# Optimization experiments

Measured on AMD Instinct MI355X. Metric: run time of the kernel, lower is better.

## Reference

```python
import jax, jax.numpy as jnp
import numpy as np

NUM_UNITS = 256
DIM_HIDDEN = 1024
NUM_GROUPS = 8
BATCH = 768
MASK_P = 0.2


def setup_inputs() -> dict:
    key = jax.random.key(0)
    k_x, k_m, k_w1, k_w2 = jax.random.split(key, 4)
    x = jax.random.normal(k_x, (BATCH, NUM_UNITS), dtype=jnp.float32)
    mask = jax.random.bernoulli(k_m, MASK_P, (BATCH, NUM_UNITS))  # True = drop unit
    # Xavier-normal initialized linear layers (zeros bias), as in _weights_init.
    s1 = float(np.sqrt(2.0 / (NUM_UNITS + DIM_HIDDEN)))
    s2 = float(np.sqrt(2.0 / (DIM_HIDDEN + NUM_UNITS)))
    W1 = jax.random.normal(k_w1, (NUM_UNITS, DIM_HIDDEN), dtype=jnp.float32) * s1
    b1 = jnp.zeros((DIM_HIDDEN,), dtype=jnp.float32)
    W2 = jax.random.normal(k_w2, (DIM_HIDDEN, NUM_UNITS), dtype=jnp.float32) * s2
    b2 = jnp.zeros((NUM_UNITS,), dtype=jnp.float32)
    temperature = jnp.ones((NUM_UNITS,), dtype=jnp.float32)
    return {"x": x, "mask": mask, "W1": W1, "b1": b1, "W2": W2, "b2": b2,
            "temperature": temperature}


def _mlp(v, W1, b1, W2, b2):
    h = jax.nn.leaky_relu(v @ W1 + b1, negative_slope=0.01)
    return h @ W2 + b2


def reference(x, mask, W1, b1, W2, b2, temperature):
    B = x.shape[0]
    key_ = _mlp(x, W1, b1, W2, b2)                      # [B, U]
    x_masked = jnp.where(mask, 0.0, x)                  # UnitMask: drop units
    query = _mlp(x_masked, W1, b1, W2, b2)              # [B, U]
    # w[i, j, u] = -|key[j,u] - query[i,u]| * temperature[u]
    w = -jnp.abs(key_[None, :, :] - query[:, None, :]) * temperature
    eye = jnp.eye(B, dtype=bool)[:, :, None]
    w = jnp.where(eye, -jnp.inf, w)
    w = w.reshape(B, B // NUM_GROUPS, NUM_GROUPS, NUM_UNITS)
    w = jax.nn.softmax(w, axis=1)
    w = w.reshape(B, B, NUM_UNITS) / 8
    return (w, mask)
```

## Files before the change

kernel.cpp:

```cpp
#include <hip/hip_runtime.h>
#include <math.h>

#define NU   256
#define DH   1024
#define NG   8
#define BB   768
#define NU4  64
#define JCH  96

typedef float nfloat4 __attribute__((ext_vector_type(4)));

__global__ __launch_bounds__(256) void build_x2(const float* __restrict__ x,
                                                const int* __restrict__ mask,
                                                float* __restrict__ X2) {
    int idx = blockIdx.x * 256 + threadIdx.x;
    int r = idx >> 8;
    int c = idx & 255;
    if (r < BB) {
        X2[idx] = x[idx];
    } else {
        int src = (r - BB) * NU + c;
        X2[idx] = mask[src] ? 0.0f : x[src];
    }
}

__global__ __launch_bounds__(256) void gemm_bias(const float* __restrict__ A,
                                                 const float* __restrict__ B,
                                                 const float* __restrict__ bias,
                                                 float* __restrict__ C,
                                                 int M, int N, int K, int leaky) {
    const int BK = 16;
    __shared__ float As[BK][64 + 1];
    __shared__ float Bs[BK][64];
    int t  = threadIdx.x;
    int tx = t & 15;
    int ty = t >> 4;
    int m0 = blockIdx.y * 64;
    int n0 = blockIdx.x * 64;

    float acc[4][4] = {};

    for (int k0 = 0; k0 < K; k0 += BK) {
        {
            int r = t >> 2;
            int c = (t & 3) * 4;
            const float4 a = *(const float4*)&A[(size_t)(m0 + r) * K + k0 + c];
            As[c + 0][r] = a.x;
            As[c + 1][r] = a.y;
            As[c + 2][r] = a.z;
            As[c + 3][r] = a.w;
        }
        {
            int r = t >> 4;
            int c = (t & 15) * 4;
            *(float4*)&Bs[r][c] = *(const float4*)&B[(size_t)(k0 + r) * N + n0 + c];
        }
        __syncthreads();
        #pragma unroll
        for (int k = 0; k < BK; ++k) {
            float a[4], b[4];
            #pragma unroll
            for (int q = 0; q < 4; ++q) a[q] = As[k][ty * 4 + q];
            #pragma unroll
            for (int q = 0; q < 4; ++q) b[q] = Bs[k][tx * 4 + q];
            #pragma unroll
            for (int im = 0; im < 4; ++im)
                #pragma unroll
                for (int in = 0; in < 4; ++in)
                    acc[im][in] = fmaf(a[im], b[in], acc[im][in]);
        }
        __syncthreads();
    }

    #pragma unroll
    for (int im = 0; im < 4; ++im) {
        int m = m0 + ty * 4 + im;
        #pragma unroll
        for (int in = 0; in < 4; ++in) {
            int n = n0 + tx * 4 + in;
            float v = acc[im][in] + bias[n];
            if (leaky) v = v > 0.0f ? v : 0.01f * v;
            C[(size_t)m * N + n] = v;
        }
    }
}

__global__ __launch_bounds__(256) void stats_kernel(const float* __restrict__ KQ,
                                                    const float* __restrict__ temp,
                                                    float* __restrict__ scale) {
    const int i  = blockIdx.x;
    const int t  = threadIdx.x;
    const int u4 = t & 63;
    const int r  = t >> 6;

    const float4* key4 = (const float4*)KQ;
    const float4* qry4 = (const float4*)(KQ + (size_t)BB * NU);
    const float4 q  = qry4[(size_t)i * NU4 + u4];
    const float4 tp = ((const float4*)temp)[u4];

    float4 sa = make_float4(0.f, 0.f, 0.f, 0.f);
    float4 sb = make_float4(0.f, 0.f, 0.f, 0.f);

    #pragma unroll 4
    for (int k = 0; k < 192; k += 2) {
        const int jA = r + 4 * k;
        const int jB = jA + 4;
        const float4 ka = key4[(size_t)jA * NU4 + u4];
        const float4 kb = key4[(size_t)jB * NU4 + u4];
        if (jA != i) {
            sa.x += __expf(-fabsf(ka.x - q.x) * tp.x);
            sa.y += __expf(-fabsf(ka.y - q.y) * tp.y);
            sa.z += __expf(-fabsf(ka.z - q.z) * tp.z);
            sa.w += __expf(-fabsf(ka.w - q.w) * tp.w);
        }
        if (jB != i) {
            sb.x += __expf(-fabsf(kb.x - q.x) * tp.x);
            sb.y += __expf(-fabsf(kb.y - q.y) * tp.y);
            sb.z += __expf(-fabsf(kb.z - q.z) * tp.z);
            sb.w += __expf(-fabsf(kb.w - q.w) * tp.w);
        }
    }

    float4 ia = make_float4(0.125f / sa.x, 0.125f / sa.y, 0.125f / sa.z, 0.125f / sa.w);
    float4 ib = make_float4(0.125f / sb.x, 0.125f / sb.y, 0.125f / sb.z, 0.125f / sb.w);
    ((float4*)scale)[((size_t)i * NG + r) * NU4 + u4]     = ia;
    ((float4*)scale)[((size_t)i * NG + r + 4) * NU4 + u4] = ib;
}

__global__ __launch_bounds__(256) void attn_write(const float* __restrict__ KQ,
                                                  const float* __restrict__ temp,
                                                  const float* __restrict__ scale,
                                                  float* __restrict__ out) {
    const int jc = blockIdx.x;
    const int i  = blockIdx.y;
    const int t  = threadIdx.x;
    const int u4 = t & 63;
    const int r  = t >> 6;
    const int j0 = jc * JCH;

    const float4* key4 = (const float4*)KQ;
    const float4* qry4 = (const float4*)(KQ + (size_t)BB * NU);
    const float4 q  = qry4[(size_t)i * NU4 + u4];
    const float4 tp = ((const float4*)temp)[u4];
    const float4 va = ((const float4*)scale)[((size_t)i * NG + r) * NU4 + u4];
    const float4 vb = ((const float4*)scale)[((size_t)i * NG + r + 4) * NU4 + u4];

    nfloat4* o4 = (nfloat4*)out + (size_t)i * BB * NU4;

    #pragma unroll 4
    for (int k = 0; k < 24; k += 2) {
        const int jA = j0 + r + 4 * k;
        const int jB = jA + 4;
        const float4 ka = key4[(size_t)jA * NU4 + u4];
        const float4 kb = key4[(size_t)jB * NU4 + u4];
        nfloat4 ea, eb;
        ea.x = __expf(-fabsf(ka.x - q.x) * tp.x) * va.x;
        ea.y = __expf(-fabsf(ka.y - q.y) * tp.y) * va.y;
        ea.z = __expf(-fabsf(ka.z - q.z) * tp.z) * va.z;
        ea.w = __expf(-fabsf(ka.w - q.w) * tp.w) * va.w;
        eb.x = __expf(-fabsf(kb.x - q.x) * tp.x) * vb.x;
        eb.y = __expf(-fabsf(kb.y - q.y) * tp.y) * vb.y;
        eb.z = __expf(-fabsf(kb.z - q.z) * tp.z) * vb.z;
        eb.w = __expf(-fabsf(kb.w - q.w) * tp.w) * vb.w;
        if (jA == i) ea = (nfloat4)0.0f;
        if (jB == i) eb = (nfloat4)0.0f;
        __builtin_nontemporal_store(ea, &o4[(size_t)jA * NU4 + u4]);
        __builtin_nontemporal_store(eb, &o4[(size_t)jB * NU4 + u4]);
    }
}

__global__ __launch_bounds__(256) void mask_out(const int* __restrict__ mask,
                                                float* __restrict__ out) {
    int idx = blockIdx.x * 256 + threadIdx.x;
    out[idx] = mask[idx] ? 1.0f : 0.0f;
}

extern "C" void kernel_launch(void* const* d_in, const int* in_sizes, int n_in,
                              void* d_out, int out_size, void* d_ws, size_t ws_size,
                              hipStream_t stream) {
    const float* x    = (const float*)d_in[0];
    const int*   mask = (const int*)d_in[1];
    const float* W1   = (const float*)d_in[2];
    const float* b1   = (const float*)d_in[3];
    const float* W2   = (const float*)d_in[4];
    const float* b2   = (const float*)d_in[5];
    const float* temp = (const float*)d_in[6];
    float* out = (float*)d_out;

    float* ws = (float*)d_ws;
    float* X2 = ws;
    float* H  = X2 + 2 * BB * NU;
    float* KQ = H + 2 * BB * DH;
    float* scale = H;

    build_x2<<<dim3(2 * BB * NU / 256), dim3(256), 0, stream>>>(x, mask, X2);

    gemm_bias<<<dim3(DH / 64, 2 * BB / 64), dim3(256), 0, stream>>>(
        X2, W1, b1, H, 2 * BB, DH, NU, 1);

    gemm_bias<<<dim3(NU / 64, 2 * BB / 64), dim3(256), 0, stream>>>(
        H, W2, b2, KQ, 2 * BB, NU, DH, 0);

    stats_kernel<<<dim3(BB), dim3(256), 0, stream>>>(KQ, temp, scale);

    attn_write<<<dim3(BB / JCH, BB), dim3(256), 0, stream>>>(KQ, temp, scale, out);

    mask_out<<<dim3(BB * NU / 256), dim3(256), 0, stream>>>(
        mask, out + (size_t)BB * BB * NU);
}
```

Measured before the change: 736.5 us.

## Fuse softmax stats and output write into one per-row kernel

Merges the normalizer kernel and the output-writing kernel so each block computes the group sums for one query row and then writes that row's outputs directly. This removes a launch and the scale buffer round-trip. In exchange the write phase runs on only one block per row instead of many chunked blocks, which lowers parallelism for the large streaming store. It also switches from nontemporal stores to regular stores.

```diff
diff --git a/kernel.cpp b/kernel.cpp
--- a/kernel.cpp
+++ b/kernel.cpp
@@ -6,9 +6,6 @@
 #define NG   8
 #define BB   768
 #define NU4  64
-#define JCH  96
-
-typedef float nfloat4 __attribute__((ext_vector_type(4)));
 
 __global__ __launch_bounds__(256) void build_x2(const float* __restrict__ x,
                                                 const int* __restrict__ mask,
@@ -85,9 +82,9 @@
     }
 }
 
-__global__ __launch_bounds__(256) void stats_kernel(const float* __restrict__ KQ,
-                                                    const float* __restrict__ temp,
-                                                    float* __restrict__ scale) {
+__global__ __launch_bounds__(256) void attn_fused(const float* __restrict__ KQ,
+                                                  const float* __restrict__ temp,
+                                                  float* __restrict__ out) {
     const int i  = blockIdx.x;
     const int t  = threadIdx.x;
     const int u4 = t & 63;
@@ -102,8 +99,8 @@
     float4 sb = make_float4(0.f, 0.f, 0.f, 0.f);
 
     #pragma unroll 4
-    for (int k = 0; k < 192; k += 2) {
-        const int jA = r + 4 * k;
+    for (int m = 0; m < 96; ++m) {
+        const int jA = r + 8 * m;
         const int jB = jA + 4;
         const float4 ka = key4[(size_t)jA * NU4 + u4];
         const float4 kb = key4[(size_t)jB * NU4 + u4];
@@ -121,51 +118,32 @@
         }
     }
 
-    float4 ia = make_float4(0.125f / sa.x, 0.125f / sa.y, 0.125f / sa.z, 0.125f / sa.w);
-    float4 ib = make_float4(0.125f / sb.x, 0.125f / sb.y, 0.125f / sb.z, 0.125f / sb.w);
-    ((float4*)scale)[((size_t)i * NG + r) * NU4 + u4]     = ia;
-    ((float4*)scale)[((size_t)i * NG + r + 4) * NU4 + u4] = ib;
-}
+    const float4 ia = make_float4(0.125f / sa.x, 0.125f / sa.y,
+                                  0.125f / sa.z, 0.125f / sa.w);
+    const float4 ib = make_float4(0.125f / sb.x, 0.125f / sb.y,
+                                  0.125f / sb.z, 0.125f / sb.w);
 
-__global__ __launch_bounds__(256) void attn_write(const float* __restrict__ KQ,
-                                                  const float* __restrict__ temp,
-                                                  const float* __restrict__ scale,
-                                                  float* __restrict__ out) {
-    const int jc = blockIdx.x;
-    const int i  = blockIdx.y;
-    const int t  = threadIdx.x;
-    const int u4 = t & 63;
-    const int r  = t >> 6;
-    const int j0 = jc * JCH;
+    float4* o4 = (float4*)out + (size_t)i * BB * NU4;
 
-    const float4* key4 = (const float4*)KQ;
-    const float4* qry4 = (const float4*)(KQ + (size_t)BB * NU);
-    const float4 q  = qry4[(size_t)i * NU4 + u4];
-    const float4 tp = ((const float4*)temp)[u4];
-    const float4 va = ((const float4*)scale)[((size_t)i * NG + r) * NU4 + u4];
-    const float4 vb = ((const float4*)scale)[((size_t)i * NG + r + 4) * NU4 + u4];
-
-    nfloat4* o4 = (nfloat4*)out + (size_t)i * BB * NU4;
-
-    #pragma unroll 4
-    for (int k = 0; k < 24; k += 2) {
-        const int jA = j0 + r + 4 * k;
+    #pragma unroll 2
+    for (int m = 0; m < 96; ++m) {
+        const int jA = r + 8 * m;
         const int jB = jA + 4;
         const float4 ka = key4[(size_t)jA * NU4 + u4];
         const float4 kb = key4[(size_t)jB * NU4 + u4];
-        nfloat4 ea, eb;
-        ea.x = __expf(-fabsf(ka.x - q.x) * tp.x) * va.x;
-        ea.y = __expf(-fabsf(ka.y - q.y) * tp.y) * va.y;
-        ea.z = __expf(-fabsf(ka.z - q.z) * tp.z) * va.z;
-        ea.w = __expf(-fabsf(ka.w - q.w) * tp.w) * va.w;
-        eb.x = __expf(-fabsf(kb.x - q.x) * tp.x) * vb.x;
-        eb.y = __expf(-fabsf(kb.y - q.y) * tp.y) * vb.y;
-        eb.z = __expf(-fabsf(kb.z - q.z) * tp.z) * vb.z;
-        eb.w = __expf(-fabsf(kb.w - q.w) * tp.w) * vb.w;
-        if (jA == i) ea = (nfloat4)0.0f;
-        if (jB == i) eb = (nfloat4)0.0f;
-        __builtin_nontemporal_store(ea, &o4[(size_t)jA * NU4 + u4]);
-        __builtin_nontemporal_store(eb, &o4[(size_t)jB * NU4 + u4]);
+        float4 ea, eb;
+        ea.x = __expf(-fabsf(ka.x - q.x) * tp.x) * ia.x;
+        ea.y = __expf(-fabsf(ka.y - q.y) * tp.y) * ia.y;
+        ea.z = __expf(-fabsf(ka.z - q.z) * tp.z) * ia.z;
+        ea.w = __expf(-fabsf(ka.w - q.w) * tp.w) * ia.w;
+        eb.x = __expf(-fabsf(kb.x - q.x) * tp.x) * ib.x;
+        eb.y = __expf(-fabsf(kb.y - q.y) * tp.y) * ib.y;
+        eb.z = __expf(-fabsf(kb.z - q.z) * tp.z) * ib.z;
+        eb.w = __expf(-fabsf(kb.w - q.w) * tp.w) * ib.w;
+        if (jA == i) ea = make_float4(0.f, 0.f, 0.f, 0.f);
+        if (jB == i) eb = make_float4(0.f, 0.f, 0.f, 0.f);
+        o4[(size_t)jA * NU4 + u4] = ea;
+        o4[(size_t)jB * NU4 + u4] = eb;
     }
 }
 
@@ -191,7 +169,6 @@
     float* X2 = ws;
     float* H  = X2 + 2 * BB * NU;
     float* KQ = H + 2 * BB * DH;
-    float* scale = H;
 
     build_x2<<<dim3(2 * BB * NU / 256), dim3(256), 0, stream>>>(x, mask, X2);
 
@@ -201,9 +178,7 @@
     gemm_bias<<<dim3(NU / 64, 2 * BB / 64), dim3(256), 0, stream>>>(
         H, W2, b2, KQ, 2 * BB, NU, DH, 0);
 
-    stats_kernel<<<dim3(BB), dim3(256), 0, stream>>>(KQ, temp, scale);
-
-    attn_write<<<dim3(BB / JCH, BB), dim3(256), 0, stream>>>(KQ, temp, scale, out);
+    attn_fused<<<dim3(BB), dim3(256), 0, stream>>>(KQ, temp, out);
 
     mask_out<<<dim3(BB * NU / 256), dim3(256), 0, stream>>>(
         mask, out + (size_t)BB * BB * NU);
```

Measured after the change: 734.5 us. No clear change (-0.3%).
